# Kernel optimization log

Hardware: AMD Instinct MI355X
Metric: run time of the kernel (lower is better)

## Reference

```python
import jax, jax.numpy as jnp
import numpy as np

N_NODES = 50000
N_EDGES = 800000
D = 128


def _gcn_norm(edge_index, edge_weights, n_nodes):
    # PyG gcn_norm with add_self_loops=True, fill_value=1.0
    src = jnp.concatenate([edge_index[0], jnp.arange(n_nodes)])
    dst = jnp.concatenate([edge_index[1], jnp.arange(n_nodes)])
    w = jnp.concatenate([edge_weights, jnp.ones((n_nodes,), edge_weights.dtype)])
    deg = jax.ops.segment_sum(w, dst, num_segments=n_nodes)
    dinv = jnp.where(deg > 0, jax.lax.rsqrt(deg), 0.0)
    norm = dinv[src] * w * dinv[dst]  # [E + N]
    return src, dst, norm


def _gcn_conv(x, src, dst, norm, W, b, n_nodes):
    h = x @ W                                   # [N, F_out]
    msg = h[src] * norm[:, None]                # gather + scale, [E+N, F_out]
    out = jax.ops.segment_sum(msg, dst, num_segments=n_nodes)
    return out + b


def setup_inputs() -> dict:
    key = jax.random.key(0)
    ks = jax.random.split(key, 12)
    s = 1.0 / np.sqrt(D)
    return {
        "x": jax.random.normal(ks[0], (N_NODES, D), jnp.float32),
        "edge_index": jax.random.randint(ks[1], (2, N_EDGES), 0, N_NODES, jnp.int64),
        "edge_weights": jax.random.uniform(ks[2], (N_EDGES,), jnp.float32),
        "W1": jax.random.normal(ks[3], (D, D), jnp.float32) * s,
        "b1": jnp.zeros((D,), jnp.float32),
        "W2": jax.random.normal(ks[4], (D, D), jnp.float32) * s,
        "b2": jnp.zeros((D,), jnp.float32),
        "W3": jax.random.normal(ks[5], (D, D), jnp.float32) * s,
        "b3": jnp.zeros((D,), jnp.float32),
        "Wl": jax.random.normal(ks[6], (D, D), jnp.float32) * s,
        "bl": jnp.zeros((D,), jnp.float32),
    }


def reference(x, edge_index, edge_weights, W1, b1, W2, b2, W3, b3, Wl, bl):
    n = x.shape[0]
    src, dst, norm = _gcn_norm(edge_index, edge_weights, n)
    h = _gcn_conv(x, src, dst, norm, W1, b1, n)
    h = jax.nn.relu(h)
    h = _gcn_conv(h, src, dst, norm, W2, b2, n)
    h = jax.nn.relu(h)
    h = _gcn_conv(h, src, dst, norm, W3, b3, n)
    # final 'linear' activation entry == nn.Linear(out_size, out_size)
    return h @ Wl + bl
```

## Files before the change

### kernel.cpp

```cpp
#include <hip/hip_runtime.h>
#include <hip/hip_fp16.h>


#define D 128
#define CNT64_STRIDE 8
#define SLOTS 64

typedef __attribute__((ext_vector_type(8))) _Float16 half8;
typedef __attribute__((ext_vector_type(4))) float floatx4;

template <bool A_IS_F32>
__device__ __forceinline__ void gemm_body(int bid, const void* Aptr,
                                          const float* W, const float* bias,
                                          float* C32, __half* C16, int N) {
    __shared__ _Float16 Wl[128][136];
    int tid = threadIdx.x;

#pragma unroll
    for (int j = 0; j < 32; j++) {
        int e = tid + j * 512;
        int k = e >> 7, n = e & 127;
        Wl[n][k] = (_Float16)W[e];
    }
    __syncthreads();

    int wave = tid >> 6, lane = tid & 63;
    int m = lane & 15, q = lane >> 4;
    int R0 = bid * 128 + wave * 16;

    const float*  A32p = (const float*)Aptr;
    const __half* A16p = (const __half*)Aptr;

    floatx4 acc[8];
#pragma unroll
    for (int ct = 0; ct < 8; ct++) acc[ct] = (floatx4){0.f, 0.f, 0.f, 0.f};

    int arow = R0 + m;
    bool rok = arow < N;

#pragma unroll
    for (int kk = 0; kk < 4; kk++) {
        half8 a = {0, 0, 0, 0, 0, 0, 0, 0};
        if (rok) {
            if (A_IS_F32) {
                const float* p = &A32p[(size_t)arow * 128 + kk * 32 + q * 8];
                float4 f0 = *(const float4*)p;
                float4 f1 = *(const float4*)(p + 4);
                a[0] = (_Float16)f0.x; a[1] = (_Float16)f0.y;
                a[2] = (_Float16)f0.z; a[3] = (_Float16)f0.w;
                a[4] = (_Float16)f1.x; a[5] = (_Float16)f1.y;
                a[6] = (_Float16)f1.z; a[7] = (_Float16)f1.w;
            } else {
                a = *(const half8*)&A16p[(size_t)arow * 128 + kk * 32 + q * 8];
            }
        }
#pragma unroll
        for (int ct = 0; ct < 8; ct++) {
            half8 b = *(const half8*)&Wl[ct * 16 + m][kk * 32 + q * 8];
            acc[ct] = __builtin_amdgcn_mfma_f32_16x16x32_f16(a, b, acc[ct], 0, 0, 0);
        }
    }

#pragma unroll
    for (int r = 0; r < 4; r++) {
        int row = R0 + q * 4 + r;
        if (row >= N) continue;
#pragma unroll
        for (int ct = 0; ct < 8; ct++) {
            int col = ct * 16 + m;
            float v = acc[ct][r];
            if (C16) C16[(size_t)row * 128 + col] = __float2half_rn(v);
            if (C32) C32[(size_t)row * 128 + col] = v + bias[col];
        }
    }
}

template <bool A_IS_F32>
__global__ __launch_bounds__(512) void k_gemm_mfma(const void* __restrict__ Aptr,
                                                   const float* __restrict__ W,
                                                   const float* __restrict__ bias,
                                                   float* __restrict__ C32,
                                                   __half* __restrict__ C16, int N) {
    gemm_body<A_IS_F32>(blockIdx.x, Aptr, W, bias, C32, C16, N);
}

__global__ __launch_bounds__(512) void k_build_gemm1(const float* __restrict__ x,
                                                     const float* __restrict__ W1,
                                                     __half* __restrict__ y16,
                                                     const int* __restrict__ dst,
                                                     const float* __restrict__ w,
                                                     unsigned long long* __restrict__ cnt8,
                                                     int* __restrict__ loc,
                                                     int N, int E, int gg, int ggp) {
    int b = (int)blockIdx.x;
    if (b < gg) {
        gemm_body<true>(b, x, W1, nullptr, nullptr, y16, N);
        return;
    }
    if (b < ggp) return;
    int e = (b - ggp) * 512 + threadIdx.x;
    if (e < E) {
        int d = dst[e];
        unsigned int wq = __float2uint_rn(w[e] * 32767.0f);
        unsigned long long old =
            atomicAdd(&cnt8[(size_t)d * CNT64_STRIDE], (1ull << 32) | (unsigned long long)wq);
        loc[e] = (int)(old >> 32);
    }
}

__global__ __launch_bounds__(256) void k_dinv(const unsigned long long* __restrict__ cnt8,
                                              float* __restrict__ dinv,
                                              int* __restrict__ cnt32, int N) {
    int i = blockIdx.x * 256 + threadIdx.x;
    if (i < N) {
        unsigned long long p = cnt8[(size_t)i * CNT64_STRIDE];
        cnt32[i] = (int)(p >> 32);
        dinv[i] = rsqrtf(1.0f + (float)(unsigned int)p * (1.0f / 32767.0f));
    }
}

__global__ __launch_bounds__(256) void k_fill(const int* __restrict__ ei,
                                              const float* __restrict__ w,
                                              const float* __restrict__ dinv,
                                              const int* __restrict__ loc,
                                              unsigned int* __restrict__ ev, int E) {
    int e = blockIdx.x * 256 + threadIdx.x;
    if (e < E) {
        int s = ei[e];
        int d = ei[E + e];
        float val = w[e] * dinv[s] * dinv[d];
        unsigned int wq = __float2uint_rn(val * 32767.0f);
        ev[(size_t)d * SLOTS + loc[e]] = (wq << 17) | (unsigned int)s;
    }
}

__device__ __forceinline__ void fma8(float acc[8], float v, uint4 q) {
    union { uint4 uu; __half2 h2[4]; } U; U.uu = q;
    float2 f0 = __half22float2(U.h2[0]);
    float2 f1 = __half22float2(U.h2[1]);
    float2 f2 = __half22float2(U.h2[2]);
    float2 f3 = __half22float2(U.h2[3]);
    acc[0] = fmaf(v, f0.x, acc[0]); acc[1] = fmaf(v, f0.y, acc[1]);
    acc[2] = fmaf(v, f1.x, acc[2]); acc[3] = fmaf(v, f1.y, acc[3]);
    acc[4] = fmaf(v, f2.x, acc[4]); acc[5] = fmaf(v, f2.y, acc[5]);
    acc[6] = fmaf(v, f3.x, acc[6]); acc[7] = fmaf(v, f3.y, acc[7]);
}

__global__ __launch_bounds__(256) void k_agg(const __half* __restrict__ y16,
                                             const int* __restrict__ cnt32,
                                             const unsigned int* __restrict__ ev,
                                             const float* __restrict__ dinv,
                                             const float* __restrict__ bias,
                                             __half* __restrict__ out16,
                                             int N, int relu) {
    int i = blockIdx.x * 4 + (threadIdx.x >> 6);
    if (i >= N) return;
    int lane = threadIdx.x & 63;
    int g = lane >> 4;
    int sl = lane & 15;

    float acc[8];
#pragma unroll
    for (int j = 0; j < 8; j++) acc[j] = 0.f;

    int cnt = cnt32[i];
    const unsigned int* evp = ev + (size_t)i * SLOTS;

    if (cnt > 0) {
        if (cnt <= 16) {
            unsigned int p[4];
            float v[4];
            uint4 q4[4];
#pragma unroll
            for (int u = 0; u < 4; u++) {
                int idx = u * 4 + g;
                bool ok = idx < cnt;
                p[u] = evp[ok ? idx : 0];
                v[u] = ok ? (float)(p[u] >> 17) * (1.0f / 32767.0f) : 0.0f;
            }
#pragma unroll
            for (int u = 0; u < 4; u++)
                q4[u] = *(const uint4*)&y16[(size_t)(p[u] & 0x1FFFFu) * D + sl * 8];
#pragma unroll
            for (int u = 0; u < 4; u++) fma8(acc, v[u], q4[u]);
        } else {
            for (int base = 0; base < cnt; base += 32) {
                unsigned int p[8];
                float v[8];
                uint4 q4[8];
#pragma unroll
                for (int u = 0; u < 8; u++) {
                    int idx = base + u * 4 + g;
                    bool ok = idx < cnt;
                    p[u] = evp[ok ? idx : 0];
                    v[u] = ok ? (float)(p[u] >> 17) * (1.0f / 32767.0f) : 0.0f;
                }
#pragma unroll
                for (int u = 0; u < 8; u++)
                    q4[u] = *(const uint4*)&y16[(size_t)(p[u] & 0x1FFFFu) * D + sl * 8];
#pragma unroll
                for (int u = 0; u < 8; u++) fma8(acc, v[u], q4[u]);
            }
        }
    }

#pragma unroll
    for (int j = 0; j < 8; j++) {
        acc[j] += __shfl_xor(acc[j], 16, 64);
        acc[j] += __shfl_xor(acc[j], 32, 64);
    }

    if (g == 0) {
        float di = dinv[i];
        float di2 = di * di;
        union { uint4 u; __half2 h2[4]; } S;
        S.u = *(const uint4*)&y16[(size_t)i * D + sl * 8];
        float2 s0 = __half22float2(S.h2[0]);
        float2 s1 = __half22float2(S.h2[1]);
        float2 s2 = __half22float2(S.h2[2]);
        float2 s3 = __half22float2(S.h2[3]);
        float4 b0 = *(const float4*)&bias[sl * 8];
        float4 b1 = *(const float4*)&bias[sl * 8 + 4];
        float o[8];
        o[0] = b0.x + acc[0] + di2 * s0.x;
        o[1] = b0.y + acc[1] + di2 * s0.y;
        o[2] = b0.z + acc[2] + di2 * s1.x;
        o[3] = b0.w + acc[3] + di2 * s1.y;
        o[4] = b1.x + acc[4] + di2 * s2.x;
        o[5] = b1.y + acc[5] + di2 * s2.y;
        o[6] = b1.z + acc[6] + di2 * s3.x;
        o[7] = b1.w + acc[7] + di2 * s3.y;
        if (relu) {
#pragma unroll
            for (int j = 0; j < 8; j++) o[j] = fmaxf(o[j], 0.f);
        }
        union { uint4 u; __half2 h2[4]; } O;
        O.h2[0] = __float22half2_rn(make_float2(o[0], o[1]));
        O.h2[1] = __float22half2_rn(make_float2(o[2], o[3]));
        O.h2[2] = __float22half2_rn(make_float2(o[4], o[5]));
        O.h2[3] = __float22half2_rn(make_float2(o[6], o[7]));
        *(uint4*)&out16[(size_t)i * D + sl * 8] = O.u;
    }
}

extern "C" void kernel_launch(void* const* d_in, const int* in_sizes, int n_in,
                              void* d_out, int out_size, void* d_ws, size_t ws_size,
                              hipStream_t stream) {
    const float* x  = (const float*)d_in[0];
    const int*   ei = (const int*)d_in[1];
    const float* ew = (const float*)d_in[2];
    const float* W1 = (const float*)d_in[3];
    const float* b1 = (const float*)d_in[4];
    const float* W2 = (const float*)d_in[5];
    const float* b2 = (const float*)d_in[6];
    const float* W3 = (const float*)d_in[7];
    const float* b3 = (const float*)d_in[8];
    const float* Wl = (const float*)d_in[9];
    const float* bl = (const float*)d_in[10];

    int N = in_sizes[0] / D;
    int E = in_sizes[2];

    char* ws = (char*)d_ws;
    size_t off = 0;
    auto alloc = [&](size_t bytes) {
        void* p = ws + off;
        off = (off + bytes + 255) & ~(size_t)255;
        return p;
    };
    unsigned long long* cnt8 = (unsigned long long*)alloc((size_t)N * 64);
    float*  dinv  = (float*)alloc((size_t)N * 4);
    int*    cnt32 = (int*)  alloc((size_t)N * 4);
    int*    loc   = (int*)  alloc((size_t)E * 4);
    unsigned int* ev = (unsigned int*)alloc((size_t)N * SLOTS * 4);
    __half* y16  = (__half*)alloc((size_t)N * D * 2);
    __half* z16  = (__half*)alloc((size_t)N * D * 2);

    int nbN    = (N + 255) / 256;
    int nbE    = (E + 255) / 256;
    int nbE512 = (E + 511) / 512;
    int gg     = (N + 127) / 128;
    int ggp    = (gg + 7) & ~7;
    int ga     = (N + 3) / 4;

    hipMemsetAsync(cnt8, 0, (size_t)N * 64, stream);
    k_build_gemm1<<<ggp + nbE512, 512, 0, stream>>>(x, W1, y16, ei + E, ew,
                                                    cnt8, loc, N, E, gg, ggp);
    k_dinv<<<nbN, 256, 0, stream>>>(cnt8, dinv, cnt32, N);
    k_fill<<<nbE, 256, 0, stream>>>(ei, ew, dinv, loc, ev, E);

    k_agg<<<ga, 256, 0, stream>>>(y16, cnt32, ev, dinv, b1, z16, N, 1);
    k_gemm_mfma<false><<<gg, 512, 0, stream>>>(z16, W2, nullptr, nullptr, y16, N);
    k_agg<<<ga, 256, 0, stream>>>(y16, cnt32, ev, dinv, b2, z16, N, 1);
    k_gemm_mfma<false><<<gg, 512, 0, stream>>>(z16, W3, nullptr, nullptr, y16, N);
    k_agg<<<ga, 256, 0, stream>>>(y16, cnt32, ev, dinv, b3, z16, N, 0);
    k_gemm_mfma<false><<<gg, 512, 0, stream>>>(z16, Wl, bl, (float*)d_out, nullptr, N);
}
```

Measured before the change: 277.9 us.

## Fuse aggregation with following GEMM and compute dinv inline

Each aggregation kernel now also runs the next layer's dense GEMM. Aggregated rows stay in shared memory as fp16 and feed MFMA directly, so the z16 intermediate never round-trips through global memory. This removes three separate GEMM launches. The standalone dinv kernel is dropped: degree normalization is recomputed from the packed count/weight word in k_fill and in the aggregator. The aggregator is also reorganized so half-waves handle a node and read edge slots in vectorized 16-entry chunks. In exchange, each block reloads and converts W into LDS, shared memory use per block is higher, and paired nodes with unequal degree do padded work.

```diff
diff --git a/kernel.cpp b/kernel.cpp
--- a/kernel.cpp
+++ b/kernel.cpp
@@ -9,18 +9,27 @@
 typedef __attribute__((ext_vector_type(8))) _Float16 half8;
 typedef __attribute__((ext_vector_type(4))) float floatx4;
 
-template <bool A_IS_F32>
-__device__ __forceinline__ void gemm_body(int bid, const void* Aptr,
-                                          const float* W, const float* bias,
-                                          float* C32, __half* C16, int N) {
+__device__ __forceinline__ void fma8(float acc[8], float v, uint4 q) {
+    union { uint4 uu; __half2 h2[4]; } U; U.uu = q;
+    float2 f0 = __half22float2(U.h2[0]);
+    float2 f1 = __half22float2(U.h2[1]);
+    float2 f2 = __half22float2(U.h2[2]);
+    float2 f3 = __half22float2(U.h2[3]);
+    acc[0] = fmaf(v, f0.x, acc[0]); acc[1] = fmaf(v, f0.y, acc[1]);
+    acc[2] = fmaf(v, f1.x, acc[2]); acc[3] = fmaf(v, f1.y, acc[3]);
+    acc[4] = fmaf(v, f2.x, acc[4]); acc[5] = fmaf(v, f2.y, acc[5]);
+    acc[6] = fmaf(v, f3.x, acc[6]); acc[7] = fmaf(v, f3.y, acc[7]);
+}
+
+__device__ __forceinline__ void gemm1_body(int bid, const float* A32p,
+                                           const float* W, __half* C16, int N) {
     __shared__ _Float16 Wl[128][136];
     int tid = threadIdx.x;
 
 #pragma unroll
     for (int j = 0; j < 32; j++) {
         int e = tid + j * 512;
-        int k = e >> 7, n = e & 127;
-        Wl[n][k] = (_Float16)W[e];
+        Wl[e & 127][e >> 7] = (_Float16)W[e];
     }
     __syncthreads();
 
@@ -28,9 +37,6 @@
     int m = lane & 15, q = lane >> 4;
     int R0 = bid * 128 + wave * 16;
 
-    const float*  A32p = (const float*)Aptr;
-    const __half* A16p = (const __half*)Aptr;
-
     floatx4 acc[8];
 #pragma unroll
     for (int ct = 0; ct < 8; ct++) acc[ct] = (floatx4){0.f, 0.f, 0.f, 0.f};
@@ -42,17 +48,13 @@
     for (int kk = 0; kk < 4; kk++) {
         half8 a = {0, 0, 0, 0, 0, 0, 0, 0};
         if (rok) {
-            if (A_IS_F32) {
-                const float* p = &A32p[(size_t)arow * 128 + kk * 32 + q * 8];
-                float4 f0 = *(const float4*)p;
-                float4 f1 = *(const float4*)(p + 4);
-                a[0] = (_Float16)f0.x; a[1] = (_Float16)f0.y;
-                a[2] = (_Float16)f0.z; a[3] = (_Float16)f0.w;
-                a[4] = (_Float16)f1.x; a[5] = (_Float16)f1.y;
-                a[6] = (_Float16)f1.z; a[7] = (_Float16)f1.w;
-            } else {
-                a = *(const half8*)&A16p[(size_t)arow * 128 + kk * 32 + q * 8];
-            }
+            const float* p = &A32p[(size_t)arow * 128 + kk * 32 + q * 8];
+            float4 f0 = *(const float4*)p;
+            float4 f1 = *(const float4*)(p + 4);
+            a[0] = (_Float16)f0.x; a[1] = (_Float16)f0.y;
+            a[2] = (_Float16)f0.z; a[3] = (_Float16)f0.w;
+            a[4] = (_Float16)f1.x; a[5] = (_Float16)f1.y;
+            a[6] = (_Float16)f1.z; a[7] = (_Float16)f1.w;
         }
 #pragma unroll
         for (int ct = 0; ct < 8; ct++) {
@@ -66,22 +68,9 @@
         int row = R0 + q * 4 + r;
         if (row >= N) continue;
 #pragma unroll
-        for (int ct = 0; ct < 8; ct++) {
-            int col = ct * 16 + m;
-            float v = acc[ct][r];
-            if (C16) C16[(size_t)row * 128 + col] = __float2half_rn(v);
-            if (C32) C32[(size_t)row * 128 + col] = v + bias[col];
-        }
-    }
-}
-
-template <bool A_IS_F32>
-__global__ __launch_bounds__(512) void k_gemm_mfma(const void* __restrict__ Aptr,
-                                                   const float* __restrict__ W,
-                                                   const float* __restrict__ bias,
-                                                   float* __restrict__ C32,
-                                                   __half* __restrict__ C16, int N) {
-    gemm_body<A_IS_F32>(blockIdx.x, Aptr, W, bias, C32, C16, N);
+        for (int ct = 0; ct < 8; ct++)
+            C16[(size_t)row * 128 + ct * 16 + m] = __float2half_rn(acc[ct][r]);
+    }
 }
 
 __global__ __launch_bounds__(512) void k_build_gemm1(const float* __restrict__ x,
@@ -94,7 +83,7 @@
                                                      int N, int E, int gg, int ggp) {
     int b = (int)blockIdx.x;
     if (b < gg) {
-        gemm_body<true>(b, x, W1, nullptr, nullptr, y16, N);
+        gemm1_body(b, x, W1, y16, N);
         return;
     }
     if (b < ggp) return;
@@ -108,138 +97,157 @@
     }
 }
 
-__global__ __launch_bounds__(256) void k_dinv(const unsigned long long* __restrict__ cnt8,
-                                              float* __restrict__ dinv,
-                                              int* __restrict__ cnt32, int N) {
-    int i = blockIdx.x * 256 + threadIdx.x;
-    if (i < N) {
-        unsigned long long p = cnt8[(size_t)i * CNT64_STRIDE];
-        cnt32[i] = (int)(p >> 32);
-        dinv[i] = rsqrtf(1.0f + (float)(unsigned int)p * (1.0f / 32767.0f));
-    }
-}
-
 __global__ __launch_bounds__(256) void k_fill(const int* __restrict__ ei,
                                               const float* __restrict__ w,
-                                              const float* __restrict__ dinv,
+                                              const unsigned int* __restrict__ wsum32,
                                               const int* __restrict__ loc,
                                               unsigned int* __restrict__ ev, int E) {
     int e = blockIdx.x * 256 + threadIdx.x;
     if (e < E) {
         int s = ei[e];
         int d = ei[E + e];
-        float val = w[e] * dinv[s] * dinv[d];
+        float dvs = rsqrtf(1.0f + (float)wsum32[(size_t)s * 16] * (1.0f / 32767.0f));
+        float dvd = rsqrtf(1.0f + (float)wsum32[(size_t)d * 16] * (1.0f / 32767.0f));
+        float val = w[e] * dvs * dvd;
         unsigned int wq = __float2uint_rn(val * 32767.0f);
         ev[(size_t)d * SLOTS + loc[e]] = (wq << 17) | (unsigned int)s;
     }
 }
 
-__device__ __forceinline__ void fma8(float acc[8], float v, uint4 q) {
-    union { uint4 uu; __half2 h2[4]; } U; U.uu = q;
-    float2 f0 = __half22float2(U.h2[0]);
-    float2 f1 = __half22float2(U.h2[1]);
-    float2 f2 = __half22float2(U.h2[2]);
-    float2 f3 = __half22float2(U.h2[3]);
-    acc[0] = fmaf(v, f0.x, acc[0]); acc[1] = fmaf(v, f0.y, acc[1]);
-    acc[2] = fmaf(v, f1.x, acc[2]); acc[3] = fmaf(v, f1.y, acc[3]);
-    acc[4] = fmaf(v, f2.x, acc[4]); acc[5] = fmaf(v, f2.y, acc[5]);
-    acc[6] = fmaf(v, f3.x, acc[6]); acc[7] = fmaf(v, f3.y, acc[7]);
-}
-
-__global__ __launch_bounds__(256) void k_agg(const __half* __restrict__ y16,
-                                             const int* __restrict__ cnt32,
-                                             const unsigned int* __restrict__ ev,
-                                             const float* __restrict__ dinv,
-                                             const float* __restrict__ bias,
-                                             __half* __restrict__ out16,
-                                             int N, int relu) {
-    int i = blockIdx.x * 4 + (threadIdx.x >> 6);
-    if (i >= N) return;
-    int lane = threadIdx.x & 63;
-    int g = lane >> 4;
-    int sl = lane & 15;
-
-    float acc[8];
-#pragma unroll
-    for (int j = 0; j < 8; j++) acc[j] = 0.f;
-
-    int cnt = cnt32[i];
-    const unsigned int* evp = ev + (size_t)i * SLOTS;
-
-    if (cnt > 0) {
-        if (cnt <= 16) {
-            unsigned int p[4];
-            float v[4];
-            uint4 q4[4];
-#pragma unroll
-            for (int u = 0; u < 4; u++) {
-                int idx = u * 4 + g;
-                bool ok = idx < cnt;
-                p[u] = evp[ok ? idx : 0];
+__global__ __launch_bounds__(512, 4) void k_agg_gemm(
+    const __half* __restrict__ yin,
+    const unsigned long long* __restrict__ cnt8,
+    const unsigned int* __restrict__ ev,
+    const float* __restrict__ bagg,
+    const float* __restrict__ W,
+    const float* __restrict__ bout,
+    float* __restrict__ C32,
+    __half* __restrict__ yout,
+    int N, int relu) {
+    __shared__ _Float16 Wl[128][136];
+    __shared__ _Float16 Z[64][136];
+    int tid = threadIdx.x;
+
+#pragma unroll
+    for (int j = 0; j < 32; j++) {
+        int e = tid + j * 512;
+        Wl[e & 127][e >> 7] = (_Float16)W[e];
+    }
+
+    int wave = tid >> 6, lane = tid & 63;
+    int h = lane >> 5;
+    int l5 = lane & 31;
+    int g2 = l5 >> 4;
+    int sl = l5 & 15;
+
+    int R0 = (int)blockIdx.x * 64;
+
+    float4 b0 = *(const float4*)&bagg[sl * 8];
+    float4 b1 = *(const float4*)&bagg[sl * 8 + 4];
+
+#pragma unroll 1
+    for (int pair = 0; pair < 4; pair++) {
+        int nloc = wave * 8 + pair * 2 + h;
+        int i = R0 + nloc;
+        bool valid = i < N;
+
+        unsigned long long pk = valid ? cnt8[(size_t)i * CNT64_STRIDE] : 0ull;
+        int cnt = (int)(pk >> 32);
+        float di = rsqrtf(1.0f + (float)(unsigned int)pk * (1.0f / 32767.0f));
+
+        const unsigned int* evp = ev + (size_t)(valid ? i : 0) * SLOTS;
+
+        float acc[8];
+#pragma unroll
+        for (int j = 0; j < 8; j++) acc[j] = 0.f;
+
+        int cntmax = max(cnt, __shfl_xor(cnt, 32, 64));
+        for (int base = 0; base < cntmax; base += 16) {
+            uint4 ea = *(const uint4*)&evp[base + g2 * 8];
+            uint4 eb = *(const uint4*)&evp[base + g2 * 8 + 4];
+            unsigned int p[8] = {ea.x, ea.y, ea.z, ea.w, eb.x, eb.y, eb.z, eb.w};
+            float v[8];
+            uint4 q4[8];
+#pragma unroll
+            for (int u = 0; u < 8; u++) {
+                bool ok = (base + g2 * 8 + u) < cnt;
                 v[u] = ok ? (float)(p[u] >> 17) * (1.0f / 32767.0f) : 0.0f;
+                int r = min((int)(p[u] & 0x1FFFFu), N - 1);
+                q4[u] = *(const uint4*)&yin[(size_t)r * D + sl * 8];
             }
 #pragma unroll
-            for (int u = 0; u < 4; u++)
-                q4[u] = *(const uint4*)&y16[(size_t)(p[u] & 0x1FFFFu) * D + sl * 8];
-#pragma unroll
-            for (int u = 0; u < 4; u++) fma8(acc, v[u], q4[u]);
-        } else {
-            for (int base = 0; base < cnt; base += 32) {
-                unsigned int p[8];
-                float v[8];
-                uint4 q4[8];
-#pragma unroll
-                for (int u = 0; u < 8; u++) {
-                    int idx = base + u * 4 + g;
-                    bool ok = idx < cnt;
-                    p[u] = evp[ok ? idx : 0];
-                    v[u] = ok ? (float)(p[u] >> 17) * (1.0f / 32767.0f) : 0.0f;
+            for (int u = 0; u < 8; u++) fma8(acc, v[u], q4[u]);
+        }
+
+#pragma unroll
+        for (int j = 0; j < 8; j++) acc[j] += __shfl_xor(acc[j], 16, 64);
+
+        if (g2 == 0) {
+            float o[8];
+            if (valid) {
+                float di2 = di * di;
+                union { uint4 u; __half2 h2[4]; } S;
+                S.u = *(const uint4*)&yin[(size_t)i * D + sl * 8];
+                float2 s0 = __half22float2(S.h2[0]);
+                float2 s1 = __half22float2(S.h2[1]);
+                float2 s2 = __half22float2(S.h2[2]);
+                float2 s3 = __half22float2(S.h2[3]);
+                o[0] = b0.x + acc[0] + di2 * s0.x;
+                o[1] = b0.y + acc[1] + di2 * s0.y;
+                o[2] = b0.z + acc[2] + di2 * s1.x;
+                o[3] = b0.w + acc[3] + di2 * s1.y;
+                o[4] = b1.x + acc[4] + di2 * s2.x;
+                o[5] = b1.y + acc[5] + di2 * s2.y;
+                o[6] = b1.z + acc[6] + di2 * s3.x;
+                o[7] = b1.w + acc[7] + di2 * s3.y;
+                if (relu) {
+#pragma unroll
+                    for (int j = 0; j < 8; j++) o[j] = fmaxf(o[j], 0.f);
                 }
-#pragma unroll
-                for (int u = 0; u < 8; u++)
-                    q4[u] = *(const uint4*)&y16[(size_t)(p[u] & 0x1FFFFu) * D + sl * 8];
-#pragma unroll
-                for (int u = 0; u < 8; u++) fma8(acc, v[u], q4[u]);
+            } else {
+#pragma unroll
+                for (int j = 0; j < 8; j++) o[j] = 0.f;
             }
-        }
-    }
-
-#pragma unroll
-    for (int j = 0; j < 8; j++) {
-        acc[j] += __shfl_xor(acc[j], 16, 64);
-        acc[j] += __shfl_xor(acc[j], 32, 64);
-    }
-
-    if (g == 0) {
-        float di = dinv[i];
-        float di2 = di * di;
-        union { uint4 u; __half2 h2[4]; } S;
-        S.u = *(const uint4*)&y16[(size_t)i * D + sl * 8];
-        float2 s0 = __half22float2(S.h2[0]);
-        float2 s1 = __half22float2(S.h2[1]);
-        float2 s2 = __half22float2(S.h2[2]);
-        float2 s3 = __half22float2(S.h2[3]);
-        float4 b0 = *(const float4*)&bias[sl * 8];
-        float4 b1 = *(const float4*)&bias[sl * 8 + 4];
-        float o[8];
-        o[0] = b0.x + acc[0] + di2 * s0.x;
-        o[1] = b0.y + acc[1] + di2 * s0.y;
-        o[2] = b0.z + acc[2] + di2 * s1.x;
-        o[3] = b0.w + acc[3] + di2 * s1.y;
-        o[4] = b1.x + acc[4] + di2 * s2.x;
-        o[5] = b1.y + acc[5] + di2 * s2.y;
-        o[6] = b1.z + acc[6] + di2 * s3.x;
-        o[7] = b1.w + acc[7] + di2 * s3.y;
-        if (relu) {
-#pragma unroll
-            for (int j = 0; j < 8; j++) o[j] = fmaxf(o[j], 0.f);
-        }
-        union { uint4 u; __half2 h2[4]; } O;
-        O.h2[0] = __float22half2_rn(make_float2(o[0], o[1]));
-        O.h2[1] = __float22half2_rn(make_float2(o[2], o[3]));
-        O.h2[2] = __float22half2_rn(make_float2(o[4], o[5]));
-        O.h2[3] = __float22half2_rn(make_float2(o[6], o[7]));
-        *(uint4*)&out16[(size_t)i * D + sl * 8] = O.u;
+            union { uint4 u; __half2 h2[4]; } O;
+            O.h2[0] = __float22half2_rn(make_float2(o[0], o[1]));
+            O.h2[1] = __float22half2_rn(make_float2(o[2], o[3]));
+            O.h2[2] = __float22half2_rn(make_float2(o[4], o[5]));
+            O.h2[3] = __float22half2_rn(make_float2(o[6], o[7]));
+            *(uint4*)&Z[nloc][sl * 8] = O.u;
+        }
+    }
+
+    __syncthreads();
+
+    int m = lane & 15, q = lane >> 4;
+    int rg = wave >> 1;
+    int ch = wave & 1;
+
+    floatx4 acc2[4];
+#pragma unroll
+    for (int ct = 0; ct < 4; ct++) acc2[ct] = (floatx4){0.f, 0.f, 0.f, 0.f};
+
+#pragma unroll
+    for (int kk = 0; kk < 4; kk++) {
+        half8 a = *(const half8*)&Z[rg * 16 + m][kk * 32 + q * 8];
+#pragma unroll
+        for (int ct = 0; ct < 4; ct++) {
+            half8 b = *(const half8*)&Wl[ch * 64 + ct * 16 + m][kk * 32 + q * 8];
+            acc2[ct] = __builtin_amdgcn_mfma_f32_16x16x32_f16(a, b, acc2[ct], 0, 0, 0);
+        }
+    }
+
+#pragma unroll
+    for (int r = 0; r < 4; r++) {
+        int row = R0 + rg * 16 + q * 4 + r;
+        if (row >= N) continue;
+#pragma unroll
+        for (int ct = 0; ct < 4; ct++) {
+            int col = ch * 64 + ct * 16 + m;
+            float v = acc2[ct][r];
+            if (yout) yout[(size_t)row * D + col] = __float2half_rn(v);
+            else      C32[(size_t)row * D + col] = v + bout[col];
+        }
     }
 }
 
@@ -269,30 +277,23 @@
         return p;
     };
     unsigned long long* cnt8 = (unsigned long long*)alloc((size_t)N * 64);
-    float*  dinv  = (float*)alloc((size_t)N * 4);
-    int*    cnt32 = (int*)  alloc((size_t)N * 4);
-    int*    loc   = (int*)  alloc((size_t)E * 4);
+    int*    loc  = (int*)alloc((size_t)E * 4);
     unsigned int* ev = (unsigned int*)alloc((size_t)N * SLOTS * 4);
-    __half* y16  = (__half*)alloc((size_t)N * D * 2);
-    __half* z16  = (__half*)alloc((size_t)N * D * 2);
-
-    int nbN    = (N + 255) / 256;
+    __half* yA   = (__half*)alloc((size_t)N * D * 2);
+    __half* yB   = (__half*)alloc((size_t)N * D * 2);
+
     int nbE    = (E + 255) / 256;
     int nbE512 = (E + 511) / 512;
     int gg     = (N + 127) / 128;
     int ggp    = (gg + 7) & ~7;
-    int ga     = (N + 3) / 4;
+    int nf     = (N + 63) / 64;
 
     hipMemsetAsync(cnt8, 0, (size_t)N * 64, stream);
-    k_build_gemm1<<<ggp + nbE512, 512, 0, stream>>>(x, W1, y16, ei + E, ew,
+    k_build_gemm1<<<ggp + nbE512, 512, 0, stream>>>(x, W1, yA, ei + E, ew,
                                                     cnt8, loc, N, E, gg, ggp);
-    k_dinv<<<nbN, 256, 0, stream>>>(cnt8, dinv, cnt32, N);
-    k_fill<<<nbE, 256, 0, stream>>>(ei, ew, dinv, loc, ev, E);
-
-    k_agg<<<ga, 256, 0, stream>>>(y16, cnt32, ev, dinv, b1, z16, N, 1);
-    k_gemm_mfma<false><<<gg, 512, 0, stream>>>(z16, W2, nullptr, nullptr, y16, N);
-    k_agg<<<ga, 256, 0, stream>>>(y16, cnt32, ev, dinv, b2, z16, N, 1);
-    k_gemm_mfma<false><<<gg, 512, 0, stream>>>(z16, W3, nullptr, nullptr, y16, N);
-    k_agg<<<ga, 256, 0, stream>>>(y16, cnt32, ev, dinv, b3, z16, N, 0);
-    k_gemm_mfma<false><<<gg, 512, 0, stream>>>(z16, Wl, bl, (float*)d_out, nullptr, N);
-}
+    k_fill<<<nbE, 256, 0, stream>>>(ei, ew, (const unsigned int*)cnt8, loc, ev, E);
+
+    k_agg_gemm<<<nf, 512, 0, stream>>>(yA, cnt8, ev, b1, W2, nullptr, nullptr, yB, N, 1);
+    k_agg_gemm<<<nf, 512, 0, stream>>>(yB, cnt8, ev, b2, W3, nullptr, nullptr, yA, N, 1);
+    k_agg_gemm<<<nf, 512, 0, stream>>>(yA, cnt8, ev, b3, Wl, bl, (float*)d_out, nullptr, N, 0);
+}
```

Measured after the change: 280.9 us. Within noise of the previous version (+1.1%).

## Fuse edge-slot fill into build kernel and defer dinv scaling to aggregation

Applied to the files above, without the earlier changes.

The build kernel now writes each edge's raw weight and source straight into the per-destination slot table with a 32-bit counter atomic, removing the separate loc array and fill kernel. A new header kernel sums the quantized weights per row to compute dinv and the counts. The aggregation applies dinv[src] per edge and dinv[dst] at the end, which adds a gather per edge in each of three layers. GEMM blocks are interleaved with edge blocks, and edges beyond 64 per node are silently dropped.

```diff
diff --git a/kernel.cpp b/kernel.cpp
--- a/kernel.cpp
+++ b/kernel.cpp
@@ -3,7 +3,7 @@
 
 
 #define D 128
-#define CNT64_STRIDE 8
+#define CNTP_STRIDE 16
 #define SLOTS 64
 
 typedef __attribute__((ext_vector_type(8))) _Float16 half8;
@@ -19,8 +19,7 @@
 #pragma unroll
     for (int j = 0; j < 32; j++) {
         int e = tid + j * 512;
-        int k = e >> 7, n = e & 127;
-        Wl[n][k] = (_Float16)W[e];
+        Wl[e & 127][e >> 7] = (_Float16)W[e];
     }
     __syncthreads();
 
@@ -87,50 +86,51 @@
 __global__ __launch_bounds__(512) void k_build_gemm1(const float* __restrict__ x,
                                                      const float* __restrict__ W1,
                                                      __half* __restrict__ y16,
-                                                     const int* __restrict__ dst,
+                                                     const int* __restrict__ ei,
                                                      const float* __restrict__ w,
-                                                     unsigned long long* __restrict__ cnt8,
-                                                     int* __restrict__ loc,
-                                                     int N, int E, int gg, int ggp) {
+                                                     unsigned int* __restrict__ cntp,
+                                                     unsigned int* __restrict__ ev,
+                                                     int N, int E, int gg, int r) {
     int b = (int)blockIdx.x;
-    if (b < gg) {
-        gemm_body<true>(b, x, W1, nullptr, nullptr, y16, N);
+    if (b % r == 0 && b / r < gg) {
+        gemm_body<true>(b / r, x, W1, nullptr, nullptr, y16, N);
         return;
     }
-    if (b < ggp) return;
-    int e = (b - ggp) * 512 + threadIdx.x;
-    if (e < E) {
-        int d = dst[e];
-        unsigned int wq = __float2uint_rn(w[e] * 32767.0f);
-        unsigned long long old =
-            atomicAdd(&cnt8[(size_t)d * CNT64_STRIDE], (1ull << 32) | (unsigned long long)wq);
-        loc[e] = (int)(old >> 32);
-    }
-}
-
-__global__ __launch_bounds__(256) void k_dinv(const unsigned long long* __restrict__ cnt8,
-                                              float* __restrict__ dinv,
-                                              int* __restrict__ cnt32, int N) {
-    int i = blockIdx.x * 256 + threadIdx.x;
-    if (i < N) {
-        unsigned long long p = cnt8[(size_t)i * CNT64_STRIDE];
-        cnt32[i] = (int)(p >> 32);
-        dinv[i] = rsqrtf(1.0f + (float)(unsigned int)p * (1.0f / 32767.0f));
-    }
-}
-
-__global__ __launch_bounds__(256) void k_fill(const int* __restrict__ ei,
-                                              const float* __restrict__ w,
-                                              const float* __restrict__ dinv,
-                                              const int* __restrict__ loc,
-                                              unsigned int* __restrict__ ev, int E) {
-    int e = blockIdx.x * 256 + threadIdx.x;
+    int ng = min(gg, (b + r - 1) / r);
+    int e = (b - ng) * 512 + threadIdx.x;
     if (e < E) {
         int s = ei[e];
         int d = ei[E + e];
-        float val = w[e] * dinv[s] * dinv[d];
-        unsigned int wq = __float2uint_rn(val * 32767.0f);
-        ev[(size_t)d * SLOTS + loc[e]] = (wq << 17) | (unsigned int)s;
+        unsigned int wq = __float2uint_rn(w[e] * 32767.0f);
+        unsigned int loc = atomicAdd(&cntp[(size_t)d * CNTP_STRIDE], 1u);
+        if (loc < SLOTS)
+            ev[(size_t)d * SLOTS + loc] = (wq << 17) | (unsigned int)s;
+    }
+}
+
+__global__ __launch_bounds__(256) void k_hdr(const unsigned int* __restrict__ cntp,
+                                             const unsigned int* __restrict__ ev,
+                                             float* __restrict__ dinv,
+                                             int* __restrict__ cnt32, int N) {
+    int i = blockIdx.x * 16 + (threadIdx.x >> 4);
+    if (i >= N) return;
+    int l = threadIdx.x & 15;
+
+    uint4 q = *(const uint4*)&ev[(size_t)i * SLOTS + l * 4];
+    int cnt = min((int)cntp[(size_t)i * CNTP_STRIDE], SLOTS);
+
+    unsigned int sum = 0;
+    int base = l * 4;
+    if (base + 0 < cnt) sum += q.x >> 17;
+    if (base + 1 < cnt) sum += q.y >> 17;
+    if (base + 2 < cnt) sum += q.z >> 17;
+    if (base + 3 < cnt) sum += q.w >> 17;
+#pragma unroll
+    for (int dlt = 1; dlt < 16; dlt <<= 1) sum += __shfl_xor(sum, dlt, 64);
+
+    if (l == 0) {
+        dinv[i] = rsqrtf(1.0f + (float)sum * (1.0f / 32767.0f));
+        cnt32[i] = cnt;
     }
 }
 
@@ -148,8 +148,8 @@
 
 __global__ __launch_bounds__(256) void k_agg(const __half* __restrict__ y16,
                                              const int* __restrict__ cnt32,
+                                             const float* __restrict__ dinv,
                                              const unsigned int* __restrict__ ev,
-                                             const float* __restrict__ dinv,
                                              const float* __restrict__ bias,
                                              __half* __restrict__ out16,
                                              int N, int relu) {
@@ -159,49 +159,49 @@
     int g = lane >> 4;
     int sl = lane & 15;
 
+    const unsigned int* evp = ev + (size_t)i * SLOTS;
+
+    int cnt = cnt32[i];
+    float di = dinv[i];
+    unsigned int p0[4];
+#pragma unroll
+    for (int u = 0; u < 4; u++) p0[u] = evp[u * 4 + g];
+
     float acc[8];
 #pragma unroll
     for (int j = 0; j < 8; j++) acc[j] = 0.f;
 
-    int cnt = cnt32[i];
-    const unsigned int* evp = ev + (size_t)i * SLOTS;
-
-    if (cnt > 0) {
-        if (cnt <= 16) {
-            unsigned int p[4];
-            float v[4];
-            uint4 q4[4];
-#pragma unroll
-            for (int u = 0; u < 4; u++) {
-                int idx = u * 4 + g;
-                bool ok = idx < cnt;
-                p[u] = evp[ok ? idx : 0];
-                v[u] = ok ? (float)(p[u] >> 17) * (1.0f / 32767.0f) : 0.0f;
-            }
-#pragma unroll
-            for (int u = 0; u < 4; u++)
-                q4[u] = *(const uint4*)&y16[(size_t)(p[u] & 0x1FFFFu) * D + sl * 8];
-#pragma unroll
-            for (int u = 0; u < 4; u++) fma8(acc, v[u], q4[u]);
-        } else {
-            for (int base = 0; base < cnt; base += 32) {
-                unsigned int p[8];
-                float v[8];
-                uint4 q4[8];
-#pragma unroll
-                for (int u = 0; u < 8; u++) {
-                    int idx = base + u * 4 + g;
-                    bool ok = idx < cnt;
-                    p[u] = evp[ok ? idx : 0];
-                    v[u] = ok ? (float)(p[u] >> 17) * (1.0f / 32767.0f) : 0.0f;
-                }
-#pragma unroll
-                for (int u = 0; u < 8; u++)
-                    q4[u] = *(const uint4*)&y16[(size_t)(p[u] & 0x1FFFFu) * D + sl * 8];
-#pragma unroll
-                for (int u = 0; u < 8; u++) fma8(acc, v[u], q4[u]);
-            }
-        }
+    {
+        float v[4]; float ds[4]; uint4 q4[4];
+#pragma unroll
+        for (int u = 0; u < 4; u++) {
+            bool ok = (u * 4 + g) < cnt;
+            int s = min((int)(p0[u] & 0x1FFFFu), N - 1);
+            v[u] = ok ? (float)(p0[u] >> 17) * (1.0f / 32767.0f) : 0.0f;
+            ds[u] = dinv[s];
+            q4[u] = *(const uint4*)&y16[(size_t)s * D + sl * 8];
+        }
+#pragma unroll
+        for (int u = 0; u < 4; u++) fma8(acc, v[u] * ds[u], q4[u]);
+    }
+
+    for (int base = 16; base < cnt; base += 32) {
+        unsigned int p[8]; float v[8]; float ds[8]; uint4 q4[8];
+#pragma unroll
+        for (int u = 0; u < 8; u++) {
+            int idx = base + u * 4 + g;
+            bool ok = idx < cnt;
+            p[u] = evp[ok ? idx : 0];
+            v[u] = ok ? (float)(p[u] >> 17) * (1.0f / 32767.0f) : 0.0f;
+        }
+#pragma unroll
+        for (int u = 0; u < 8; u++) {
+            int s = min((int)(p[u] & 0x1FFFFu), N - 1);
+            ds[u] = dinv[s];
+            q4[u] = *(const uint4*)&y16[(size_t)s * D + sl * 8];
+        }
+#pragma unroll
+        for (int u = 0; u < 8; u++) fma8(acc, v[u] * ds[u], q4[u]);
     }
 
 #pragma unroll
@@ -211,7 +211,6 @@
     }
 
     if (g == 0) {
-        float di = dinv[i];
         float di2 = di * di;
         union { uint4 u; __half2 h2[4]; } S;
         S.u = *(const uint4*)&y16[(size_t)i * D + sl * 8];
@@ -222,14 +221,14 @@
         float4 b0 = *(const float4*)&bias[sl * 8];
         float4 b1 = *(const float4*)&bias[sl * 8 + 4];
         float o[8];
-        o[0] = b0.x + acc[0] + di2 * s0.x;
-        o[1] = b0.y + acc[1] + di2 * s0.y;
-        o[2] = b0.z + acc[2] + di2 * s1.x;
-        o[3] = b0.w + acc[3] + di2 * s1.y;
-        o[4] = b1.x + acc[4] + di2 * s2.x;
-        o[5] = b1.y + acc[5] + di2 * s2.y;
-        o[6] = b1.z + acc[6] + di2 * s3.x;
-        o[7] = b1.w + acc[7] + di2 * s3.y;
+        o[0] = b0.x + di * acc[0] + di2 * s0.x;
+        o[1] = b0.y + di * acc[1] + di2 * s0.y;
+        o[2] = b0.z + di * acc[2] + di2 * s1.x;
+        o[3] = b0.w + di * acc[3] + di2 * s1.y;
+        o[4] = b1.x + di * acc[4] + di2 * s2.x;
+        o[5] = b1.y + di * acc[5] + di2 * s2.y;
+        o[6] = b1.z + di * acc[6] + di2 * s3.x;
+        o[7] = b1.w + di * acc[7] + di2 * s3.y;
         if (relu) {
 #pragma unroll
             for (int j = 0; j < 8; j++) o[j] = fmaxf(o[j], 0.f);
@@ -268,31 +267,28 @@
         off = (off + bytes + 255) & ~(size_t)255;
         return p;
     };
-    unsigned long long* cnt8 = (unsigned long long*)alloc((size_t)N * 64);
-    float*  dinv  = (float*)alloc((size_t)N * 4);
-    int*    cnt32 = (int*)  alloc((size_t)N * 4);
-    int*    loc   = (int*)  alloc((size_t)E * 4);
-    unsigned int* ev = (unsigned int*)alloc((size_t)N * SLOTS * 4);
-    __half* y16  = (__half*)alloc((size_t)N * D * 2);
-    __half* z16  = (__half*)alloc((size_t)N * D * 2);
-
-    int nbN    = (N + 255) / 256;
-    int nbE    = (E + 255) / 256;
-    int nbE512 = (E + 511) / 512;
-    int gg     = (N + 127) / 128;
-    int ggp    = (gg + 7) & ~7;
-    int ga     = (N + 3) / 4;
-
-    hipMemsetAsync(cnt8, 0, (size_t)N * 64, stream);
-    k_build_gemm1<<<ggp + nbE512, 512, 0, stream>>>(x, W1, y16, ei + E, ew,
-                                                    cnt8, loc, N, E, gg, ggp);
-    k_dinv<<<nbN, 256, 0, stream>>>(cnt8, dinv, cnt32, N);
-    k_fill<<<nbE, 256, 0, stream>>>(ei, ew, dinv, loc, ev, E);
-
-    k_agg<<<ga, 256, 0, stream>>>(y16, cnt32, ev, dinv, b1, z16, N, 1);
-    k_gemm_mfma<false><<<gg, 512, 0, stream>>>(z16, W2, nullptr, nullptr, y16, N);
-    k_agg<<<ga, 256, 0, stream>>>(y16, cnt32, ev, dinv, b2, z16, N, 1);
-    k_gemm_mfma<false><<<gg, 512, 0, stream>>>(z16, W3, nullptr, nullptr, y16, N);
-    k_agg<<<ga, 256, 0, stream>>>(y16, cnt32, ev, dinv, b3, z16, N, 0);
-    k_gemm_mfma<false><<<gg, 512, 0, stream>>>(z16, Wl, bl, (float*)d_out, nullptr, N);
-}
+    unsigned int* cntp = (unsigned int*)alloc((size_t)N * 64);
+    unsigned int* ev   = (unsigned int*)alloc((size_t)N * SLOTS * 4 + 256);
+    float* dinv  = (float*)alloc((size_t)N * 4);
+    int*   cnt32 = (int*)  alloc((size_t)N * 4);
+    __half* yA   = (__half*)alloc((size_t)N * D * 2);
+    __half* yB   = (__half*)alloc((size_t)N * D * 2);
+
+    int gg = (N + 127) / 128;
+    int ne = (E + 511) / 512;
+    int T  = gg + ne;
+    int r  = (T + gg - 1) / gg;
+    int nh = (N + 15) / 16;
+    int ga = (N + 3) / 4;
+
+    hipMemsetAsync(cntp, 0, (size_t)N * 64, stream);
+    k_build_gemm1<<<T, 512, 0, stream>>>(x, W1, yA, ei, ew, cntp, ev, N, E, gg, r);
+    k_hdr<<<nh, 256, 0, stream>>>(cntp, ev, dinv, cnt32, N);
+
+    k_agg<<<ga, 256, 0, stream>>>(yA, cnt32, dinv, ev, b1, yB, N, 1);
+    k_gemm_mfma<false><<<gg, 512, 0, stream>>>(yB, W2, nullptr, nullptr, yA, N);
+    k_agg<<<ga, 256, 0, stream>>>(yA, cnt32, dinv, ev, b2, yB, N, 1);
+    k_gemm_mfma<false><<<gg, 512, 0, stream>>>(yB, W3, nullptr, nullptr, yA, N);
+    k_agg<<<ga, 256, 0, stream>>>(yA, cnt32, dinv, ev, b3, yB, N, 0);
+    k_gemm_mfma<false><<<gg, 512, 0, stream>>>(yB, Wl, bl, (float*)d_out, nullptr, N);
+}
```

Measured after the change: 308.9 us. +11.2%, slower.

## Bank degree atomics across four counters and fold dinv into fill and aggregate

Applied to the files above, without the earlier changes.

Each node's degree/count atomic is split into four banks, indexed by the low bits of the edge id, to reduce contention on hot destination counters. Slot positions become a bank prefix sum plus the local index. The separate k_dinv kernel is removed, so fill and aggregate recompute dinv and the count from the four banks. The aggregate kernel also prefetches the first 16 edge slots unconditionally and merges the small and large paths. This adds extra scattered reads of the counters per edge and per node, a four-times larger memset, and drops edges beyond 64 slots instead of overflowing.

```diff
diff --git a/kernel.cpp b/kernel.cpp
--- a/kernel.cpp
+++ b/kernel.cpp
@@ -3,8 +3,8 @@
 
 
 #define D 128
-#define CNT64_STRIDE 8
 #define SLOTS 64
+#define NBANK 4
 
 typedef __attribute__((ext_vector_type(8))) _Float16 half8;
 typedef __attribute__((ext_vector_type(4))) float floatx4;
@@ -19,8 +19,7 @@
 #pragma unroll
     for (int j = 0; j < 32; j++) {
         int e = tid + j * 512;
-        int k = e >> 7, n = e & 127;
-        Wl[n][k] = (_Float16)W[e];
+        Wl[e & 127][e >> 7] = (_Float16)W[e];
     }
     __syncthreads();
 
@@ -89,48 +88,61 @@
                                                      __half* __restrict__ y16,
                                                      const int* __restrict__ dst,
                                                      const float* __restrict__ w,
-                                                     unsigned long long* __restrict__ cnt8,
+                                                     unsigned long long* __restrict__ cntb,
                                                      int* __restrict__ loc,
-                                                     int N, int E, int gg, int ggp) {
+                                                     int N, int E, int gg) {
     int b = (int)blockIdx.x;
     if (b < gg) {
         gemm_body<true>(b, x, W1, nullptr, nullptr, y16, N);
         return;
     }
-    if (b < ggp) return;
-    int e = (b - ggp) * 512 + threadIdx.x;
+    int e = (b - gg) * 512 + threadIdx.x;
     if (e < E) {
         int d = dst[e];
+        int bank = e & (NBANK - 1);
         unsigned int wq = __float2uint_rn(w[e] * 32767.0f);
         unsigned long long old =
-            atomicAdd(&cnt8[(size_t)d * CNT64_STRIDE], (1ull << 32) | (unsigned long long)wq);
+            atomicAdd(&cntb[((size_t)d * NBANK + bank) * 8],
+                      (1ull << 32) | (unsigned long long)wq);
         loc[e] = (int)(old >> 32);
-    }
-}
-
-__global__ __launch_bounds__(256) void k_dinv(const unsigned long long* __restrict__ cnt8,
-                                              float* __restrict__ dinv,
-                                              int* __restrict__ cnt32, int N) {
-    int i = blockIdx.x * 256 + threadIdx.x;
-    if (i < N) {
-        unsigned long long p = cnt8[(size_t)i * CNT64_STRIDE];
-        cnt32[i] = (int)(p >> 32);
-        dinv[i] = rsqrtf(1.0f + (float)(unsigned int)p * (1.0f / 32767.0f));
     }
 }
 
 __global__ __launch_bounds__(256) void k_fill(const int* __restrict__ ei,
                                               const float* __restrict__ w,
-                                              const float* __restrict__ dinv,
+                                              const unsigned long long* __restrict__ cntb,
                                               const int* __restrict__ loc,
                                               unsigned int* __restrict__ ev, int E) {
     int e = blockIdx.x * 256 + threadIdx.x;
     if (e < E) {
         int s = ei[e];
         int d = ei[E + e];
-        float val = w[e] * dinv[s] * dinv[d];
+        int bank = e & (NBANK - 1);
+
+        unsigned long long s0 = cntb[((size_t)s * NBANK + 0) * 8];
+        unsigned long long s1 = cntb[((size_t)s * NBANK + 1) * 8];
+        unsigned long long s2 = cntb[((size_t)s * NBANK + 2) * 8];
+        unsigned long long s3 = cntb[((size_t)s * NBANK + 3) * 8];
+        unsigned long long d0 = cntb[((size_t)d * NBANK + 0) * 8];
+        unsigned long long d1 = cntb[((size_t)d * NBANK + 1) * 8];
+        unsigned long long d2 = cntb[((size_t)d * NBANK + 2) * 8];
+        unsigned long long d3 = cntb[((size_t)d * NBANK + 3) * 8];
+
+        unsigned int ws = (unsigned int)s0 + (unsigned int)s1 +
+                          (unsigned int)s2 + (unsigned int)s3;
+        unsigned int wd = (unsigned int)d0 + (unsigned int)d1 +
+                          (unsigned int)d2 + (unsigned int)d3;
+        float dvs = rsqrtf(1.0f + (float)ws * (1.0f / 32767.0f));
+        float dvd = rsqrtf(1.0f + (float)wd * (1.0f / 32767.0f));
+
+        int c0 = (int)(d0 >> 32), c1 = (int)(d1 >> 32), c2 = (int)(d2 >> 32);
+        int prefix = (bank > 0 ? c0 : 0) + (bank > 1 ? c1 : 0) + (bank > 2 ? c2 : 0);
+        int fin = prefix + loc[e];
+
+        float val = w[e] * dvs * dvd;
         unsigned int wq = __float2uint_rn(val * 32767.0f);
-        ev[(size_t)d * SLOTS + loc[e]] = (wq << 17) | (unsigned int)s;
+        if (fin < SLOTS)
+            ev[(size_t)d * SLOTS + fin] = (wq << 17) | (unsigned int)s;
     }
 }
 
@@ -147,9 +159,8 @@
 }
 
 __global__ __launch_bounds__(256) void k_agg(const __half* __restrict__ y16,
-                                             const int* __restrict__ cnt32,
+                                             const unsigned long long* __restrict__ cntb,
                                              const unsigned int* __restrict__ ev,
-                                             const float* __restrict__ dinv,
                                              const float* __restrict__ bias,
                                              __half* __restrict__ out16,
                                              int N, int relu) {
@@ -159,49 +170,53 @@
     int g = lane >> 4;
     int sl = lane & 15;
 
+    const unsigned int* evp = ev + (size_t)i * SLOTS;
+
+    unsigned long long h0 = cntb[((size_t)i * NBANK + 0) * 8];
+    unsigned long long h1 = cntb[((size_t)i * NBANK + 1) * 8];
+    unsigned long long h2 = cntb[((size_t)i * NBANK + 2) * 8];
+    unsigned long long h3 = cntb[((size_t)i * NBANK + 3) * 8];
+    unsigned int p0[4];
+#pragma unroll
+    for (int u = 0; u < 4; u++) p0[u] = evp[u * 4 + g];
+
+    int cnt = (int)((h0 >> 32) + (h1 >> 32) + (h2 >> 32) + (h3 >> 32));
+    cnt = min(cnt, SLOTS);
+    unsigned int wsum = (unsigned int)h0 + (unsigned int)h1 +
+                        (unsigned int)h2 + (unsigned int)h3;
+    float di = rsqrtf(1.0f + (float)wsum * (1.0f / 32767.0f));
+
     float acc[8];
 #pragma unroll
     for (int j = 0; j < 8; j++) acc[j] = 0.f;
 
-    int cnt = cnt32[i];
-    const unsigned int* evp = ev + (size_t)i * SLOTS;
-
-    if (cnt > 0) {
-        if (cnt <= 16) {
-            unsigned int p[4];
-            float v[4];
-            uint4 q4[4];
-#pragma unroll
-            for (int u = 0; u < 4; u++) {
-                int idx = u * 4 + g;
-                bool ok = idx < cnt;
-                p[u] = evp[ok ? idx : 0];
-                v[u] = ok ? (float)(p[u] >> 17) * (1.0f / 32767.0f) : 0.0f;
-            }
-#pragma unroll
-            for (int u = 0; u < 4; u++)
-                q4[u] = *(const uint4*)&y16[(size_t)(p[u] & 0x1FFFFu) * D + sl * 8];
-#pragma unroll
-            for (int u = 0; u < 4; u++) fma8(acc, v[u], q4[u]);
-        } else {
-            for (int base = 0; base < cnt; base += 32) {
-                unsigned int p[8];
-                float v[8];
-                uint4 q4[8];
-#pragma unroll
-                for (int u = 0; u < 8; u++) {
-                    int idx = base + u * 4 + g;
-                    bool ok = idx < cnt;
-                    p[u] = evp[ok ? idx : 0];
-                    v[u] = ok ? (float)(p[u] >> 17) * (1.0f / 32767.0f) : 0.0f;
-                }
-#pragma unroll
-                for (int u = 0; u < 8; u++)
-                    q4[u] = *(const uint4*)&y16[(size_t)(p[u] & 0x1FFFFu) * D + sl * 8];
-#pragma unroll
-                for (int u = 0; u < 8; u++) fma8(acc, v[u], q4[u]);
-            }
-        }
+    {
+        float v[4]; uint4 q4[4];
+#pragma unroll
+        for (int u = 0; u < 4; u++) {
+            bool ok = (u * 4 + g) < cnt;
+            v[u] = ok ? (float)(p0[u] >> 17) * (1.0f / 32767.0f) : 0.0f;
+            int s = min((int)(p0[u] & 0x1FFFFu), N - 1);
+            q4[u] = *(const uint4*)&y16[(size_t)s * D + sl * 8];
+        }
+#pragma unroll
+        for (int u = 0; u < 4; u++) fma8(acc, v[u], q4[u]);
+    }
+
+    for (int base = 16; base < cnt; base += 32) {
+        unsigned int p[8]; float v[8]; uint4 q4[8];
+#pragma unroll
+        for (int u = 0; u < 8; u++) {
+            int idx = base + u * 4 + g;
+            bool ok = idx < cnt;
+            p[u] = evp[ok ? idx : 0];
+            v[u] = ok ? (float)(p[u] >> 17) * (1.0f / 32767.0f) : 0.0f;
+        }
+#pragma unroll
+        for (int u = 0; u < 8; u++)
+            q4[u] = *(const uint4*)&y16[(size_t)(p[u] & 0x1FFFFu) * D + sl * 8];
+#pragma unroll
+        for (int u = 0; u < 8; u++) fma8(acc, v[u], q4[u]);
     }
 
 #pragma unroll
@@ -211,7 +226,6 @@
     }
 
     if (g == 0) {
-        float di = dinv[i];
         float di2 = di * di;
         union { uint4 u; __half2 h2[4]; } S;
         S.u = *(const uint4*)&y16[(size_t)i * D + sl * 8];
@@ -268,31 +282,26 @@
         off = (off + bytes + 255) & ~(size_t)255;
         return p;
     };
-    unsigned long long* cnt8 = (unsigned long long*)alloc((size_t)N * 64);
-    float*  dinv  = (float*)alloc((size_t)N * 4);
-    int*    cnt32 = (int*)  alloc((size_t)N * 4);
-    int*    loc   = (int*)  alloc((size_t)E * 4);
+    unsigned long long* cntb = (unsigned long long*)alloc((size_t)N * NBANK * 64);
+    int*    loc  = (int*)alloc((size_t)E * 4);
     unsigned int* ev = (unsigned int*)alloc((size_t)N * SLOTS * 4);
-    __half* y16  = (__half*)alloc((size_t)N * D * 2);
-    __half* z16  = (__half*)alloc((size_t)N * D * 2);
-
-    int nbN    = (N + 255) / 256;
+    __half* yA   = (__half*)alloc((size_t)N * D * 2);
+    __half* yB   = (__half*)alloc((size_t)N * D * 2);
+
     int nbE    = (E + 255) / 256;
     int nbE512 = (E + 511) / 512;
     int gg     = (N + 127) / 128;
-    int ggp    = (gg + 7) & ~7;
     int ga     = (N + 3) / 4;
 
-    hipMemsetAsync(cnt8, 0, (size_t)N * 64, stream);
-    k_build_gemm1<<<ggp + nbE512, 512, 0, stream>>>(x, W1, y16, ei + E, ew,
-                                                    cnt8, loc, N, E, gg, ggp);
-    k_dinv<<<nbN, 256, 0, stream>>>(cnt8, dinv, cnt32, N);
-    k_fill<<<nbE, 256, 0, stream>>>(ei, ew, dinv, loc, ev, E);
-
-    k_agg<<<ga, 256, 0, stream>>>(y16, cnt32, ev, dinv, b1, z16, N, 1);
-    k_gemm_mfma<false><<<gg, 512, 0, stream>>>(z16, W2, nullptr, nullptr, y16, N);
-    k_agg<<<ga, 256, 0, stream>>>(y16, cnt32, ev, dinv, b2, z16, N, 1);
-    k_gemm_mfma<false><<<gg, 512, 0, stream>>>(z16, W3, nullptr, nullptr, y16, N);
-    k_agg<<<ga, 256, 0, stream>>>(y16, cnt32, ev, dinv, b3, z16, N, 0);
-    k_gemm_mfma<false><<<gg, 512, 0, stream>>>(z16, Wl, bl, (float*)d_out, nullptr, N);
-}
+    hipMemsetAsync(cntb, 0, (size_t)N * NBANK * 64, stream);
+    k_build_gemm1<<<gg + nbE512, 512, 0, stream>>>(x, W1, yA, ei + E, ew,
+                                                   cntb, loc, N, E, gg);
+    k_fill<<<nbE, 256, 0, stream>>>(ei, ew, cntb, loc, ev, E);
+
+    k_agg<<<ga, 256, 0, stream>>>(yA, cntb, ev, b1, yB, N, 1);
+    k_gemm_mfma<false><<<gg, 512, 0, stream>>>(yB, W2, nullptr, nullptr, yA, N);
+    k_agg<<<ga, 256, 0, stream>>>(yA, cntb, ev, b2, yB, N, 1);
+    k_gemm_mfma<false><<<gg, 512, 0, stream>>>(yB, W3, nullptr, nullptr, yA, N);
+    k_agg<<<ga, 256, 0, stream>>>(yA, cntb, ev, b3, yB, N, 0);
+    k_gemm_mfma<false><<<gg, 512, 0, stream>>>(yB, Wl, bl, (float*)d_out, nullptr, N);
+}
```

New measurement: 328.5 us. 1.18x slower.
